# Performance work log

Hardware: AMD Instinct MI355X
Metric: run time of the kernel (lower is better)

Reference implementation:

```python
import jax, jax.numpy as jnp
import numpy as np

N, F_IN, E = 50000, 128, 800000
D1, D2, D3, NUM_LAYERS = 90, 80, 50, 4
EPS = 1e-5


def _gcn_norm(edge_index, n):
    # add self-loops, compute symmetric normalization deg^{-1/2} A_hat deg^{-1/2}
    loops = jnp.arange(n, dtype=edge_index.dtype)
    src = jnp.concatenate([edge_index[0], loops])
    dst = jnp.concatenate([edge_index[1], loops])
    deg = jax.ops.segment_sum(jnp.ones_like(src, dtype=jnp.float32), dst, num_segments=n)
    deg_isqrt = jnp.where(deg > 0, jax.lax.rsqrt(deg), 0.0)
    norm = deg_isqrt[src] * deg_isqrt[dst]  # [E+N]
    return src, dst, norm


def _gcn_conv(x, w, b, src, dst, norm, n):
    h = x @ w                                   # [N, d_out] dense transform first
    msg = h[src] * norm[:, None]                # gather + scale  [E+N, d_out]
    out = jax.ops.segment_sum(msg, dst, num_segments=n)  # scatter-add
    return out + b


def _bn(x, gamma, beta):
    # batch-statistics BatchNorm1d over node dim
    mu = jnp.mean(x, axis=0)
    var = jnp.var(x, axis=0)
    return (x - mu) * jax.lax.rsqrt(var + EPS) * gamma + beta


def setup_inputs() -> dict:
    key = jax.random.key(0)
    ks = jax.random.split(key, 16)
    s = lambda *sh: 1.0 / np.sqrt(sh[0])
    inp = {
        'x': jax.random.normal(ks[0], (N, F_IN), jnp.float32),
        'edge_index': jax.random.randint(ks[1], (2, E), 0, N, dtype=jnp.int32),
        'conv1_w': jax.random.normal(ks[2], (F_IN, D1), jnp.float32) * s(F_IN),
        'conv1_b': jnp.zeros((D1,), jnp.float32),
        'convs_w': jax.random.normal(ks[3], (NUM_LAYERS - 1, D1, D1), jnp.float32) * s(D1),
        'convs_b': jnp.zeros((NUM_LAYERS - 1, D1), jnp.float32),
        'bn1_g': jnp.ones((D1,), jnp.float32), 'bn1_b': jnp.zeros((D1,), jnp.float32),
        'fc1_w': jax.random.normal(ks[4], (D1, D2), jnp.float32) * s(D1),
        'fc1_b': jnp.zeros((D2,), jnp.float32),
        'bn2_g': jnp.ones((D2,), jnp.float32), 'bn2_b': jnp.zeros((D2,), jnp.float32),
        'fc2_w': jax.random.normal(ks[5], (D2, D3), jnp.float32) * s(D2),
        'fc2_b': jnp.zeros((D3,), jnp.float32),
        'bn3_g': jnp.ones((D3,), jnp.float32), 'bn3_b': jnp.zeros((D3,), jnp.float32),
        'fc3_w': jax.random.normal(ks[6], (D3, 1), jnp.float32) * s(D3),
        'fc3_b': jnp.zeros((1,), jnp.float32),
    }
    return inp


def reference(x, edge_index, conv1_w, conv1_b, convs_w, convs_b,
              bn1_g, bn1_b, fc1_w, fc1_b, bn2_g, bn2_b,
              fc2_w, fc2_b, bn3_g, bn3_b, fc3_w, fc3_b):
    n = x.shape[0]
    src, dst, norm = _gcn_norm(edge_index, n)
    h = jax.nn.relu(_gcn_conv(x, conv1_w, conv1_b, src, dst, norm, n))
    for i in range(convs_w.shape[0]):
        h = jax.nn.relu(_gcn_conv(h, convs_w[i], convs_b[i], src, dst, norm, n))
        h = _bn(h, bn1_g, bn1_b)
        # dropout is identity in eval mode
    h = jax.nn.relu(_bn(h @ fc1_w + fc1_b, bn2_g, bn2_b))
    h = jax.nn.relu(_bn(h @ fc2_w + fc2_b, bn3_g, bn3_b))
    return h @ fc3_w + fc3_b
```

## Files before the change

### kernel.cpp

```cpp
#include <hip/hip_runtime.h>

#define NBLK(n, b) (((n) + (b) - 1) / (b))

#define FS 96
#define FS4 24

typedef _Float16 half8_t __attribute__((ext_vector_type(8)));
typedef float float8_t __attribute__((ext_vector_type(8)));
typedef float f32x4_t __attribute__((ext_vector_type(4)));


__global__ void count_k(const int* __restrict__ dst, int* __restrict__ cnt, int e) {
  int i = blockIdx.x * blockDim.x + threadIdx.x;
  if (i < e) atomicAdd(&cnt[dst[i]], 1);
}

__global__ void isq_k(const int* __restrict__ cnt, float* __restrict__ isq, int n) {
  int i = blockIdx.x * blockDim.x + threadIdx.x;
  if (i < n) isq[i] = rsqrtf((float)cnt[i] + 1.0f);
}

__global__ __launch_bounds__(256) void scan1_k(const int* __restrict__ cnt,
                                               int* __restrict__ rowptr,
                                               int* __restrict__ partials, int n) {
  __shared__ int ls[256];
  const int t = threadIdx.x;
  const int base = blockIdx.x * 1024 + t * 4;
  int v0 = 0, v1 = 0, v2 = 0, v3 = 0;
  if (base + 3 < n) {
    int4 q = *reinterpret_cast<const int4*>(cnt + base);
    v0 = q.x; v1 = q.y; v2 = q.z; v3 = q.w;
  } else {
    if (base < n) v0 = cnt[base];
    if (base + 1 < n) v1 = cnt[base + 1];
    if (base + 2 < n) v2 = cnt[base + 2];
  }
  int s = v0 + v1 + v2 + v3;
  ls[t] = s;
  __syncthreads();
  for (int off = 1; off < 256; off <<= 1) {
    int u = (t >= off) ? ls[t - off] : 0;
    __syncthreads();
    ls[t] += u;
    __syncthreads();
  }
  int p = ls[t] - s;
  if (t == 255) partials[blockIdx.x] = ls[255];
  if (base < n) rowptr[base] = p;
  p += v0;
  if (base + 1 < n) rowptr[base + 1] = p;
  p += v1;
  if (base + 2 < n) rowptr[base + 2] = p;
  p += v2;
  if (base + 3 < n) rowptr[base + 3] = p;
}

__global__ __launch_bounds__(256) void scan2_k(const int* __restrict__ partials,
                                               int* __restrict__ offsets, int B) {
  __shared__ int ls[256];
  const int t = threadIdx.x;
  int v = (t < B) ? partials[t] : 0;
  ls[t] = v;
  __syncthreads();
  for (int off = 1; off < 256; off <<= 1) {
    int u = (t >= off) ? ls[t - off] : 0;
    __syncthreads();
    ls[t] += u;
    __syncthreads();
  }
  if (t < B) offsets[t] = ls[t] - v;
  if (t == B - 1) offsets[B] = ls[t];
}

__global__ __launch_bounds__(256) void scan3_k(int* __restrict__ rowptr,
                                               int* __restrict__ cursor,
                                               const int* __restrict__ offsets,
                                               int n, int B) {
  const int t = threadIdx.x;
  const int base = blockIdx.x * 1024 + t * 4;
  const int off = offsets[blockIdx.x];
  if (base + 3 < n) {
    int4 q = *reinterpret_cast<const int4*>(rowptr + base);
    q.x += off; q.y += off; q.z += off; q.w += off;
    *reinterpret_cast<int4*>(rowptr + base) = q;
    *reinterpret_cast<int4*>(cursor + base) = q;
  } else {
    for (int i = base; i < n; ++i) {
      int v = rowptr[i] + off;
      rowptr[i] = v;
      cursor[i] = v;
    }
  }
  if (base == 0 && blockIdx.x == 0) rowptr[n] = offsets[B];
}

__global__ void fill_k(const int* __restrict__ src, const int* __restrict__ dst,
                       int* __restrict__ cursor, unsigned short* __restrict__ csr, int e) {
  int i = blockIdx.x * blockDim.x + threadIdx.x;
  if (i >= e) return;
  int pos = atomicAdd(&cursor[dst[i]], 1);
  csr[pos] = (unsigned short)src[i];
}


template <int K, int KP, int M, int INS, int OUTS, int XF, int EPI>
__global__ __launch_bounds__(256, 2) void gemm4_k(
    const float* __restrict__ X, const float* __restrict__ W,
    const float* __restrict__ bias, const float* __restrict__ isq,
    const float* __restrict__ scale, const float* __restrict__ shift,
    void* __restrict__ OUT, int n) {
  constexpr int KG = KP / 8;
  __shared__ _Float16 Wh[6 * KG * 16 * 8];
  const int t = threadIdx.x;
  for (int idx = t; idx < KP * 96; idx += 256) {
    const int k = idx / 96, c = idx - k * 96;
    const float v = (k < K && c < M) ? W[k * M + c] : 0.0f;
    const int tt = c >> 4, cc = c & 15;
    Wh[((tt * KG + (k >> 3)) * 16 + cc) * 8 + (k & 7)] = (_Float16)v;
  }
  __syncthreads();
  const int wid = t >> 6;
  const int lane = t & 63;
  const int lr = lane & 15;
  const int hk = lane >> 4;
  const int r0 = blockIdx.x * 64 + wid * 16;
  const int arow = min(r0 + lr, n - 1);
  const float* __restrict__ xp = X + (size_t)arow * INS;
  const half8_t* __restrict__ Whv = reinterpret_cast<const half8_t*>(Wh);
  f32x4_t acc[6];
#pragma unroll
  for (int tt = 0; tt < 6; ++tt) acc[tt] = (f32x4_t){0.0f, 0.0f, 0.0f, 0.0f};
  for (int ks = 0; ks < KP; ks += 32) {
    const int kb = ks + hk * 8;
    float a[8];
    {
      float4 v0 = *reinterpret_cast<const float4*>(xp + kb);
      float4 v1 = *reinterpret_cast<const float4*>(xp + kb + 4);
      a[0] = v0.x; a[1] = v0.y; a[2] = v0.z; a[3] = v0.w;
      a[4] = v1.x; a[5] = v1.y; a[6] = v1.z; a[7] = v1.w;
    }
    if constexpr (XF == 1) {
#pragma unroll
      for (int i = 0; i < 8; ++i) a[i] = fmaxf(a[i], 0.0f);
    } else if constexpr (XF == 2 || XF == 3) {
      float4 s0 = *reinterpret_cast<const float4*>(scale + kb);
      float4 s1 = *reinterpret_cast<const float4*>(scale + kb + 4);
      float4 h0 = *reinterpret_cast<const float4*>(shift + kb);
      float4 h1 = *reinterpret_cast<const float4*>(shift + kb + 4);
      const float sc[8] = {s0.x, s0.y, s0.z, s0.w, s1.x, s1.y, s1.z, s1.w};
      const float sh[8] = {h0.x, h0.y, h0.z, h0.w, h1.x, h1.y, h1.z, h1.w};
#pragma unroll
      for (int i = 0; i < 8; ++i) {
        if constexpr (XF == 2) a[i] = fmaxf(a[i], 0.0f) * sc[i] + sh[i];
        else a[i] = fmaxf(a[i] * sc[i] + sh[i], 0.0f);
      }
    }
    half8_t af;
#pragma unroll
    for (int i = 0; i < 8; ++i) af[i] = (_Float16)a[i];
    const int kg = kb >> 3;
#pragma unroll
    for (int tt = 0; tt < 6; ++tt) {
      half8_t bf = Whv[(tt * KG + kg) * 16 + lr];
      acc[tt] = __builtin_amdgcn_mfma_f32_16x16x32_f16(af, bf, acc[tt], 0, 0, 0);
    }
  }
  const int rg = r0 + (hk << 2);
  if constexpr (EPI == 0) {
    float siq[4];
#pragma unroll
    for (int j = 0; j < 4; ++j) siq[j] = (rg + j < n) ? isq[rg + j] : 0.0f;
    _Float16* Hh = (_Float16*)OUT;
#pragma unroll
    for (int tt = 0; tt < 6; ++tt) {
      const int c = tt * 16 + lr;
      const int tb = c / 48;
      const int so = c % 48;
#pragma unroll
      for (int j = 0; j < 4; ++j) {
        const int row = rg + j;
        if (row < n)
          Hh[(size_t)tb * n * 48 + (size_t)row * 48 + so] =
              (_Float16)(acc[tt][j] * siq[j]);
      }
    }
  } else {
    float* O = (float*)OUT;
#pragma unroll
    for (int tt = 0; tt < 6; ++tt) {
      const int c = tt * 16 + lr;
      const float bv = (c < M) ? bias[c] : 0.0f;
#pragma unroll
      for (int j = 0; j < 4; ++j) {
        const int row = rg + j;
        if (row < n) O[(size_t)row * OUTS + c] = acc[tt][j] + bv;
      }
    }
  }
}


template <int K, int KP, int M, int MH, int INS, int OUTS, int XF, int EPI>
__global__ __launch_bounds__(256, 2) void gemm2_k(
    const float* __restrict__ X, const float* __restrict__ W,
    const float* __restrict__ bias, const float* __restrict__ isq,
    const float* __restrict__ scale, const float* __restrict__ shift,
    void* __restrict__ OUT, int n) {
  __shared__ float Ws[KP * MH];
  __shared__ float Sc[(XF >= 2) ? KP : 1];
  __shared__ float Sh[(XF >= 2) ? KP : 1];
  const int ms = blockIdx.y;
  for (int idx = threadIdx.x; idx < KP * MH; idx += 256) {
    int k = idx / MH;
    int m = idx - k * MH;
    int col = ms * MH + m;
    Ws[idx] = (k < K && col < M) ? W[k * M + col] : 0.0f;
  }
  if constexpr (XF >= 2) {
    for (int k = threadIdx.x; k < KP; k += 256) {
      Sc[k] = (k < K) ? scale[k] : 0.0f;
      Sh[k] = (k < K) ? shift[k] : 0.0f;
    }
  }
  __syncthreads();
  const int row = blockIdx.x * 256 + threadIdx.x;
  const bool valid = row < n;
  const float* xp = X + (size_t)(valid ? row : 0) * INS;
  float acc[MH];
#pragma unroll
  for (int m = 0; m < MH; ++m) acc[m] = 0.0f;
  for (int k0 = 0; k0 < KP; k0 += 4) {
    float4 tt = *reinterpret_cast<const float4*>(xp + k0);
    float xv[4] = {tt.x, tt.y, tt.z, tt.w};
#pragma unroll
    for (int j = 0; j < 4; ++j) {
      float xval = xv[j];
      if constexpr (XF == 1) xval = fmaxf(xval, 0.0f);
      if constexpr (XF == 2) xval = fmaxf(xval, 0.0f) * Sc[k0 + j] + Sh[k0 + j];
      if constexpr (XF == 3) xval = fmaxf(xval * Sc[k0 + j] + Sh[k0 + j], 0.0f);
      const float* wrow = &Ws[(k0 + j) * MH];
#pragma unroll
      for (int m = 0; m < MH; ++m) acc[m] += xval * wrow[m];
    }
  }
  if (!valid) return;
  float* O = (float*)OUT;
  const size_t base = (size_t)row * OUTS + ms * MH;
#pragma unroll
  for (int m = 0; m < MH; ++m) O[base + m] = acc[m] + bias[ms * MH + m];
}


__global__ __launch_bounds__(256, 6) void gather_k(
    const _Float16* __restrict__ H, const int* __restrict__ rowptr,
    const unsigned short* __restrict__ csr, const float* __restrict__ isq,
    const float* __restrict__ bias, float* __restrict__ A, int n) {
  const int wid = threadIdx.x >> 6;
  const int lane = threadIdx.x & 63;
  const int d = blockIdx.x * 4 + wid;
  if (d >= n) return;
  const int g = lane >> 4;
  const int s = lane & 15;
  const int beg = rowptr[d];
  const int end = rowptr[d + 1];
  const half8_t* __restrict__ Hp = reinterpret_cast<const half8_t*>(H);
  const int sl = (s < 6) ? s : (s - 6);
  const half8_t* __restrict__ lanebase = Hp + ((s < 6) ? 0 : (size_t)n * 6) + sl;
  float8_t acc = {0, 0, 0, 0, 0, 0, 0, 0};
  float8_t acc2 = {0, 0, 0, 0, 0, 0, 0, 0};
  if (lane < 12)
    acc += __builtin_convertvector(lanebase[(size_t)d * 6], float8_t);
  int r = beg + g;
  for (; r + 4 < end; r += 8) {
    const int v0 = (int)csr[r];
    const int v1 = (int)csr[r + 4];
    if (s < 12) {
      acc += __builtin_convertvector(lanebase[(size_t)v0 * 6], float8_t);
      acc2 += __builtin_convertvector(lanebase[(size_t)v1 * 6], float8_t);
    }
  }
  for (; r < end; r += 4) {
    const int v = (int)csr[r];
    if (s < 12) acc += __builtin_convertvector(lanebase[(size_t)v * 6], float8_t);
  }
  acc += acc2;
#pragma unroll
  for (int i = 0; i < 8; ++i) acc[i] += __shfl_xor(acc[i], 16);
#pragma unroll
  for (int i = 0; i < 8; ++i) acc[i] += __shfl_xor(acc[i], 32);
  if (lane < 12) {
    const float sc = isq[d];
    const int c = lane * 8;
    float o[8];
#pragma unroll
    for (int i = 0; i < 8; ++i)
      o[i] = acc[i] * sc + ((c + i < 90) ? bias[c + i] : 0.0f);
    float4* Ap = reinterpret_cast<float4*>(A + (size_t)d * FS + c);
    Ap[0] = make_float4(o[0], o[1], o[2], o[3]);
    Ap[1] = make_float4(o[4], o[5], o[6], o[7]);
  }
}


template <int M, bool RELU>
__global__ __launch_bounds__(256) void bn_stats4_k(const float* __restrict__ X,
                                                   float* __restrict__ gsum,
                                                   float* __restrict__ gsq, int n) {
  __shared__ float ssum[FS];
  __shared__ float ssq[FS];
  for (int i = threadIdx.x; i < FS; i += 256) { ssum[i] = 0.0f; ssq[i] = 0.0f; }
  __syncthreads();
  const int t = threadIdx.x;
  const int cq = t % FS4;
  const int rl = t / FS4;
  constexpr int ROWS = 256 / FS4;
  const float4* __restrict__ Xp = reinterpret_cast<const float4*>(X);
  if (rl < ROWS) {
    float s0 = 0, s1 = 0, s2 = 0, s3 = 0, q0 = 0, q1 = 0, q2 = 0, q3 = 0;
    for (int r = blockIdx.x * ROWS + rl; r < n; r += gridDim.x * ROWS) {
      float4 v = Xp[(size_t)r * FS4 + cq];
      if (RELU) {
        v.x = fmaxf(v.x, 0.0f); v.y = fmaxf(v.y, 0.0f);
        v.z = fmaxf(v.z, 0.0f); v.w = fmaxf(v.w, 0.0f);
      }
      s0 += v.x; q0 += v.x * v.x;
      s1 += v.y; q1 += v.y * v.y;
      s2 += v.z; q2 += v.z * v.z;
      s3 += v.w; q3 += v.w * v.w;
    }
    const int c = cq * 4;
    if (c + 0 < M) { atomicAdd(&ssum[c + 0], s0); atomicAdd(&ssq[c + 0], q0); }
    if (c + 1 < M) { atomicAdd(&ssum[c + 1], s1); atomicAdd(&ssq[c + 1], q1); }
    if (c + 2 < M) { atomicAdd(&ssum[c + 2], s2); atomicAdd(&ssq[c + 2], q2); }
    if (c + 3 < M) { atomicAdd(&ssum[c + 3], s3); atomicAdd(&ssq[c + 3], q3); }
  }
  __syncthreads();
  for (int i = threadIdx.x; i < M; i += 256) {
    atomicAdd(&gsum[i], ssum[i]);
    atomicAdd(&gsq[i], ssq[i]);
  }
}


template <int M>
__global__ void bn_final_k(const float* __restrict__ gsum, const float* __restrict__ gsq,
                           const float* __restrict__ g, const float* __restrict__ b,
                           float* __restrict__ scale, float* __restrict__ shift, float invn) {
  int c = threadIdx.x;
  if (c >= FS) return;
  if (c >= M) { scale[c] = 0.0f; shift[c] = 0.0f; return; }
  float mu = gsum[c] * invn;
  float var = gsq[c] * invn - mu * mu;
  float r = rsqrtf(var + 1e-5f);
  float sc = g[c] * r;
  scale[c] = sc;
  shift[c] = b[c] - mu * sc;
}


extern "C" void kernel_launch(void* const* d_in, const int* in_sizes, int n_in,
                              void* d_out, int out_size, void* d_ws, size_t ws_size,
                              hipStream_t stream) {
  const float* x = (const float*)d_in[0];
  const int* ei = (const int*)d_in[1];
  const float* conv1_w = (const float*)d_in[2];
  const float* conv1_b = (const float*)d_in[3];
  const float* convs_w = (const float*)d_in[4];
  const float* convs_b = (const float*)d_in[5];
  const float* bn1_g = (const float*)d_in[6];
  const float* bn1_b = (const float*)d_in[7];
  const float* fc1_w = (const float*)d_in[8];
  const float* fc1_b = (const float*)d_in[9];
  const float* bn2_g = (const float*)d_in[10];
  const float* bn2_b = (const float*)d_in[11];
  const float* fc2_w = (const float*)d_in[12];
  const float* fc2_b = (const float*)d_in[13];
  const float* bn3_g = (const float*)d_in[14];
  const float* bn3_b = (const float*)d_in[15];
  const float* fc3_w = (const float*)d_in[16];
  const float* fc3_b = (const float*)d_in[17];

  const int N = in_sizes[0] / 128;
  const int E = in_sizes[1] / 2;
  const int* src = ei;
  const int* dst = ei + E;
  const int B = NBLK(N, 1024);

  float* ws = (float*)d_ws;
  float* isq = ws;
  int* rowptr = (int*)(ws + 50048);
  int* cursor = rowptr + 50048;
  int* cnt = cursor + 50048;
  unsigned short* csr16 = (unsigned short*)(cnt + 50048);
  int* partials = (int*)(csr16 + 800000);
  int* offsets = partials + 64;
  float* stats = (float*)(offsets + 128);
  float* scale = stats + 5 * 192;
  float* shift = scale + 96;
  float* bufH = shift + 96;
  float* bufA = bufH + (size_t)N * FS;
  _Float16* bufHh = (_Float16*)bufH;

  float* gs0 = stats + 0 * 192; float* gq0 = gs0 + 96;
  float* gs1 = stats + 1 * 192; float* gq1 = gs1 + 96;
  float* gs2 = stats + 2 * 192; float* gq2 = gs2 + 96;
  float* gs3 = stats + 3 * 192; float* gq3 = gs3 + 96;
  float* gs4 = stats + 4 * 192; float* gq4 = gs4 + 96;

  hipMemsetAsync(cnt, 0, 50048 * sizeof(int), stream);
  hipMemsetAsync(stats, 0, 5 * 192 * sizeof(float), stream);
  count_k<<<NBLK(E, 256), 256, 0, stream>>>(dst, cnt, E);
  isq_k<<<NBLK(N, 256), 256, 0, stream>>>(cnt, isq, N);
  scan1_k<<<B, 256, 0, stream>>>(cnt, rowptr, partials, N);
  scan2_k<<<1, 256, 0, stream>>>(partials, offsets, B);
  scan3_k<<<B, 256, 0, stream>>>(rowptr, cursor, offsets, N, B);
  fill_k<<<NBLK(E, 256), 256, 0, stream>>>(src, dst, cursor, csr16, E);

  const int grows = NBLK(N, 256);
  const int gmf = NBLK(N, 64);
  const int ggath = NBLK(N, 4);
  const float invn = 1.0f / (float)N;

  gemm4_k<128, 128, 90, 128, FS, 0, 0><<<gmf, 256, 0, stream>>>(
      x, conv1_w, nullptr, isq, nullptr, nullptr, bufHh, N);
  gather_k<<<ggath, 256, 0, stream>>>(bufHh, rowptr, csr16, isq, conv1_b, bufA, N);

  gemm4_k<90, 96, 90, FS, FS, 1, 0><<<gmf, 256, 0, stream>>>(
      bufA, convs_w, nullptr, isq, nullptr, nullptr, bufHh, N);
  gather_k<<<ggath, 256, 0, stream>>>(bufHh, rowptr, csr16, isq, convs_b, bufA, N);
  bn_stats4_k<90, true><<<512, 256, 0, stream>>>(bufA, gs0, gq0, N);
  bn_final_k<90><<<1, 128, 0, stream>>>(gs0, gq0, bn1_g, bn1_b, scale, shift, invn);

  gemm4_k<90, 96, 90, FS, FS, 2, 0><<<gmf, 256, 0, stream>>>(
      bufA, convs_w + 90 * 90, nullptr, isq, scale, shift, bufHh, N);
  gather_k<<<ggath, 256, 0, stream>>>(bufHh, rowptr, csr16, isq, convs_b + 90, bufA, N);
  bn_stats4_k<90, true><<<512, 256, 0, stream>>>(bufA, gs1, gq1, N);
  bn_final_k<90><<<1, 128, 0, stream>>>(gs1, gq1, bn1_g, bn1_b, scale, shift, invn);

  gemm4_k<90, 96, 90, FS, FS, 2, 0><<<gmf, 256, 0, stream>>>(
      bufA, convs_w + 2 * 90 * 90, nullptr, isq, scale, shift, bufHh, N);
  gather_k<<<ggath, 256, 0, stream>>>(bufHh, rowptr, csr16, isq, convs_b + 2 * 90, bufA, N);
  bn_stats4_k<90, true><<<512, 256, 0, stream>>>(bufA, gs2, gq2, N);
  bn_final_k<90><<<1, 128, 0, stream>>>(gs2, gq2, bn1_g, bn1_b, scale, shift, invn);

  gemm4_k<90, 96, 80, FS, FS, 2, 1><<<gmf, 256, 0, stream>>>(
      bufA, fc1_w, fc1_b, nullptr, scale, shift, bufH, N);
  bn_stats4_k<80, false><<<512, 256, 0, stream>>>(bufH, gs3, gq3, N);
  bn_final_k<80><<<1, 128, 0, stream>>>(gs3, gq3, bn2_g, bn2_b, scale, shift, invn);

  gemm2_k<80, 80, 50, 25, FS, FS, 3, 1><<<dim3(grows, 2), 256, 0, stream>>>(
      bufH, fc2_w, fc2_b, nullptr, scale, shift, bufA, N);
  bn_stats4_k<50, false><<<512, 256, 0, stream>>>(bufA, gs4, gq4, N);
  bn_final_k<50><<<1, 128, 0, stream>>>(gs4, gq4, bn3_g, bn3_b, scale, shift, invn);

  gemm2_k<50, 52, 1, 1, FS, 1, 3, 1><<<dim3(grows, 1), 256, 0, stream>>>(
      bufA, fc3_w, fc3_b, nullptr, scale, shift, (float*)d_out, N);
}
```

Measured before the change: 500.5 us.

## Fuse BatchNorm statistics into gather kernel and use row-major fp16 H layout

The separate bn_stats pass after each of the three middle aggregations is folded into the gather kernel: each block accumulates ReLU'd sums and squared sums in shared memory via atomics and then adds them to global accumulators. This removes a full re-read of the 50000x96 activation buffer per layer, plus one launch. The fp16 intermediate H also switches from two 48-wide column slabs to a single 96-wide row-major layout, so each gathered neighbor row is one contiguous 192-byte segment. The cost is heavy shared and global atomic contention: 12 lanes per node, with only four nodes per block, feeding 90 global atomic pairs per block across about 12500 blocks.

```diff
diff --git a/kernel.cpp b/kernel.cpp
--- a/kernel.cpp
+++ b/kernel.cpp
@@ -174,14 +174,11 @@
 #pragma unroll
     for (int tt = 0; tt < 6; ++tt) {
       const int c = tt * 16 + lr;
-      const int tb = c / 48;
-      const int so = c % 48;
 #pragma unroll
       for (int j = 0; j < 4; ++j) {
         const int row = rg + j;
         if (row < n)
-          Hh[(size_t)tb * n * 48 + (size_t)row * 48 + so] =
-              (_Float16)(acc[tt][j] * siq[j]);
+          Hh[(size_t)row * 96 + c] = (_Float16)(acc[tt][j] * siq[j]);
       }
     }
   } else {
@@ -251,53 +248,76 @@
 }
 
 
+template <bool STATS>
 __global__ __launch_bounds__(256, 6) void gather_k(
     const _Float16* __restrict__ H, const int* __restrict__ rowptr,
     const unsigned short* __restrict__ csr, const float* __restrict__ isq,
-    const float* __restrict__ bias, float* __restrict__ A, int n) {
+    const float* __restrict__ bias, float* __restrict__ A,
+    float* __restrict__ gsum, float* __restrict__ gsq, int n) {
+  __shared__ float ssum[STATS ? FS : 1];
+  __shared__ float ssq[STATS ? FS : 1];
+  if constexpr (STATS) {
+    for (int i = threadIdx.x; i < FS; i += 256) { ssum[i] = 0.0f; ssq[i] = 0.0f; }
+    __syncthreads();
+  }
   const int wid = threadIdx.x >> 6;
   const int lane = threadIdx.x & 63;
   const int d = blockIdx.x * 4 + wid;
-  if (d >= n) return;
-  const int g = lane >> 4;
-  const int s = lane & 15;
-  const int beg = rowptr[d];
-  const int end = rowptr[d + 1];
-  const half8_t* __restrict__ Hp = reinterpret_cast<const half8_t*>(H);
-  const int sl = (s < 6) ? s : (s - 6);
-  const half8_t* __restrict__ lanebase = Hp + ((s < 6) ? 0 : (size_t)n * 6) + sl;
-  float8_t acc = {0, 0, 0, 0, 0, 0, 0, 0};
-  float8_t acc2 = {0, 0, 0, 0, 0, 0, 0, 0};
-  if (lane < 12)
-    acc += __builtin_convertvector(lanebase[(size_t)d * 6], float8_t);
-  int r = beg + g;
-  for (; r + 4 < end; r += 8) {
-    const int v0 = (int)csr[r];
-    const int v1 = (int)csr[r + 4];
-    if (s < 12) {
-      acc += __builtin_convertvector(lanebase[(size_t)v0 * 6], float8_t);
-      acc2 += __builtin_convertvector(lanebase[(size_t)v1 * 6], float8_t);
-    }
-  }
-  for (; r < end; r += 4) {
-    const int v = (int)csr[r];
-    if (s < 12) acc += __builtin_convertvector(lanebase[(size_t)v * 6], float8_t);
-  }
-  acc += acc2;
-#pragma unroll
-  for (int i = 0; i < 8; ++i) acc[i] += __shfl_xor(acc[i], 16);
-#pragma unroll
-  for (int i = 0; i < 8; ++i) acc[i] += __shfl_xor(acc[i], 32);
-  if (lane < 12) {
-    const float sc = isq[d];
-    const int c = lane * 8;
-    float o[8];
-#pragma unroll
-    for (int i = 0; i < 8; ++i)
-      o[i] = acc[i] * sc + ((c + i < 90) ? bias[c + i] : 0.0f);
-    float4* Ap = reinterpret_cast<float4*>(A + (size_t)d * FS + c);
-    Ap[0] = make_float4(o[0], o[1], o[2], o[3]);
-    Ap[1] = make_float4(o[4], o[5], o[6], o[7]);
+  if (d < n) {
+    const int g = lane >> 4;
+    const int s = lane & 15;
+    const int beg = rowptr[d];
+    const int end = rowptr[d + 1];
+    const half8_t* __restrict__ Hp = reinterpret_cast<const half8_t*>(H);
+    const half8_t* __restrict__ lanebase = Hp + ((s < 12) ? s : 0);
+    float8_t acc = {0, 0, 0, 0, 0, 0, 0, 0};
+    float8_t acc2 = {0, 0, 0, 0, 0, 0, 0, 0};
+    if (lane < 12)
+      acc += __builtin_convertvector(lanebase[(size_t)d * 12], float8_t);
+    int r = beg + g;
+    for (; r + 4 < end; r += 8) {
+      const int v0 = (int)csr[r];
+      const int v1 = (int)csr[r + 4];
+      if (s < 12) {
+        acc += __builtin_convertvector(lanebase[(size_t)v0 * 12], float8_t);
+        acc2 += __builtin_convertvector(lanebase[(size_t)v1 * 12], float8_t);
+      }
+    }
+    for (; r < end; r += 4) {
+      const int v = (int)csr[r];
+      if (s < 12) acc += __builtin_convertvector(lanebase[(size_t)v * 12], float8_t);
+    }
+    acc += acc2;
+#pragma unroll
+    for (int i = 0; i < 8; ++i) acc[i] += __shfl_xor(acc[i], 16);
+#pragma unroll
+    for (int i = 0; i < 8; ++i) acc[i] += __shfl_xor(acc[i], 32);
+    if (lane < 12) {
+      const float sc = isq[d];
+      const int c = lane * 8;
+      float o[8];
+#pragma unroll
+      for (int i = 0; i < 8; ++i)
+        o[i] = acc[i] * sc + ((c + i < 90) ? bias[c + i] : 0.0f);
+      float4* Ap = reinterpret_cast<float4*>(A + (size_t)d * FS + c);
+      Ap[0] = make_float4(o[0], o[1], o[2], o[3]);
+      Ap[1] = make_float4(o[4], o[5], o[6], o[7]);
+      if constexpr (STATS) {
+#pragma unroll
+        for (int i = 0; i < 8; ++i) {
+          const float v = fmaxf(o[i], 0.0f);
+          atomicAdd(&ssum[c + i], v);
+          atomicAdd(&ssq[c + i], v * v);
+        }
+      }
+    }
+  }
+  if constexpr (STATS) {
+    __syncthreads();
+    for (int i = threadIdx.x; i < 90; i += 256) {
+      atomicAdd(&gsum[i], ssum[i]);
+      atomicAdd(&gsq[i], ssq[i]);
+    }
   }
 }
 
@@ -423,24 +443,25 @@
 
   gemm4_k<128, 128, 90, 128, FS, 0, 0><<<gmf, 256, 0, stream>>>(
       x, conv1_w, nullptr, isq, nullptr, nullptr, bufHh, N);
-  gather_k<<<ggath, 256, 0, stream>>>(bufHh, rowptr, csr16, isq, conv1_b, bufA, N);
+  gather_k<false><<<ggath, 256, 0, stream>>>(bufHh, rowptr, csr16, isq, conv1_b,
+                                             bufA, nullptr, nullptr, N);
 
   gemm4_k<90, 96, 90, FS, FS, 1, 0><<<gmf, 256, 0, stream>>>(
       bufA, convs_w, nullptr, isq, nullptr, nullptr, bufHh, N);
-  gather_k<<<ggath, 256, 0, stream>>>(bufHh, rowptr, csr16, isq, convs_b, bufA, N);
-  bn_stats4_k<90, true><<<512, 256, 0, stream>>>(bufA, gs0, gq0, N);
+  gather_k<true><<<ggath, 256, 0, stream>>>(bufHh, rowptr, csr16, isq, convs_b,
+                                            bufA, gs0, gq0, N);
   bn_final_k<90><<<1, 128, 0, stream>>>(gs0, gq0, bn1_g, bn1_b, scale, shift, invn);
 
   gemm4_k<90, 96, 90, FS, FS, 2, 0><<<gmf, 256, 0, stream>>>(
       bufA, convs_w + 90 * 90, nullptr, isq, scale, shift, bufHh, N);
-  gather_k<<<ggath, 256, 0, stream>>>(bufHh, rowptr, csr16, isq, convs_b + 90, bufA, N);
-  bn_stats4_k<90, true><<<512, 256, 0, stream>>>(bufA, gs1, gq1, N);
+  gather_k<true><<<ggath, 256, 0, stream>>>(bufHh, rowptr, csr16, isq, convs_b + 90,
+                                            bufA, gs1, gq1, N);
   bn_final_k<90><<<1, 128, 0, stream>>>(gs1, gq1, bn1_g, bn1_b, scale, shift, invn);
 
   gemm4_k<90, 96, 90, FS, FS, 2, 0><<<gmf, 256, 0, stream>>>(
       bufA, convs_w + 2 * 90 * 90, nullptr, isq, scale, shift, bufHh, N);
-  gather_k<<<ggath, 256, 0, stream>>>(bufHh, rowptr, csr16, isq, convs_b + 2 * 90, bufA, N);
-  bn_stats4_k<90, true><<<512, 256, 0, stream>>>(bufA, gs2, gq2, N);
+  gather_k<true><<<ggath, 256, 0, stream>>>(bufHh, rowptr, csr16, isq, convs_b + 2 * 90,
+                                            bufA, gs2, gq2, N);
   bn_final_k<90><<<1, 128, 0, stream>>>(gs2, gq2, bn1_g, bn1_b, scale, shift, invn);
 
   gemm4_k<90, 96, 80, FS, FS, 2, 1><<<gmf, 256, 0, stream>>>(
```

After: 1.262 ms. 152% more time.
